# Kernel optimization log

Hardware: AMD Instinct MI355X
Metric: run time of the kernel (lower is better)

## Reference

```python
import jax, jax.numpy as jnp
import numpy as np

STRIDE = 2
PADDING = (1, 1)
OUT_PADDING = (0, 0)


def conv_transpose2d(x, weight, bias, stride, padding, out_padding):
    # weight: (Cin, Cout, kh, kw) -- torch ConvTranspose2d layout.
    # The original code does: stride-insert zeros, zero-pad by (k-1), append
    # out_padding rows/cols, valid-conv with the spatially-flipped kernel,
    # then crop `padding` from each side. That is exactly a dilated conv:
    kh, kw = weight.shape[2], weight.shape[3]
    w = jnp.flip(weight, (2, 3)).transpose(1, 0, 2, 3)  # (Cout, Cin, kh, kw)
    pad = ((kh - 1 - padding[0], kh - 1 - padding[0] + out_padding[0]),
           (kw - 1 - padding[1], kw - 1 - padding[1] + out_padding[1]))
    out = jax.lax.conv_general_dilated(
        x, w,
        window_strides=(1, 1),
        padding=pad,
        lhs_dilation=(stride, stride),
        dimension_numbers=('NCHW', 'OIHW', 'NCHW'))
    return out + bias[None, :, None, None]


def setup_inputs() -> dict:
    key = jax.random.key(0)
    k1, k2, k3 = jax.random.split(key, 3)
    Cin, Cout, kh, kw = 256, 128, 4, 4
    bnd = (1.0 / (Cin * kh * kw)) ** 0.5  # matches uniform_(-k**0.5, k**0.5)
    x = jax.random.normal(k1, (16, Cin, 64, 64), dtype=jnp.float32)
    weight = jax.random.uniform(k2, (Cin, Cout, kh, kw), jnp.float32, -bnd, bnd)
    bias = jax.random.uniform(k3, (Cout,), jnp.float32, -bnd, bnd)
    return {"x": x, "weight": weight, "bias": bias}


def reference(x, weight, bias):
    # Output: (16, 128, 128, 128) = (H-1)*2 - 2*1 + 4
    return conv_transpose2d(x, weight, bias, STRIDE, PADDING, OUT_PADDING)
```

## Files before the change

### kernel.cpp

```cpp
#include <hip/hip_runtime.h>
#include <stdint.h>

typedef unsigned short u16;
typedef __bf16 bf16x8 __attribute__((ext_vector_type(8)));
typedef float f32x4 __attribute__((ext_vector_type(4)));

static const size_t XT_BYTES = (size_t)16 * 66 * 66 * 256 * 2;
static const size_t WK_BYTES = (size_t)2 * 4 * 8 * 2 * 128 * 32 * 2;

__device__ __forceinline__ u16 f2bf(float f) {
  unsigned u = __float_as_uint(f);
  unsigned r = (u + 0x7fff + ((u >> 16) & 1)) >> 16;
  return (u16)r;
}

__device__ __forceinline__ void ld_g2l16(const u16* g, void* l) {
  __builtin_amdgcn_global_load_lds(
      (const __attribute__((address_space(1))) unsigned int*)(uintptr_t)g,
      (__attribute__((address_space(3))) unsigned int*)(unsigned int)(uintptr_t)l,
      16, 0, 0);
}

__device__ __forceinline__ int swz4(int row) { return (row ^ (row >> 2)) & 3; }

__global__ __launch_bounds__(256) void prep_x(const float* __restrict__ x,
                                              u16* __restrict__ xt) {
  __shared__ __align__(16) u16 sh[64 * 264];
  const int t = threadIdx.x;
  const int ihp = blockIdx.x;
  const int n = blockIdx.y;
  u16* xtn = xt + ((size_t)(n * 66 + ihp)) * 66 * 256;
  if (ihp == 0 || ihp == 65) {
    for (int j = 0; j < 9; ++j) {
      int idx = j * 256 + t;
      if (idx < 2112) ((uint4*)xtn)[idx] = make_uint4(0, 0, 0, 0);
    }
    return;
  }
  const int ih = ihp - 1;
  const int iw0 = (t & 15) * 4;
  const int cib = t >> 4;
  const float* xb = x + (size_t)n * 1048576 + (size_t)ih * 64;
#pragma unroll
  for (int it = 0; it < 16; ++it) {
    int ci = it * 16 + cib;
    const float4 v = *(const float4*)(xb + (size_t)ci * 4096 + iw0);
    sh[(iw0 + 0) * 264 + ci] = f2bf(v.x);
    sh[(iw0 + 1) * 264 + ci] = f2bf(v.y);
    sh[(iw0 + 2) * 264 + ci] = f2bf(v.z);
    sh[(iw0 + 3) * 264 + ci] = f2bf(v.w);
  }
  __syncthreads();
#pragma unroll
  for (int j = 0; j < 8; ++j) {
    int idx = j * 256 + t;
    int iw = idx >> 5;
    int chunk = idx & 31;
    uint4 v = *(const uint4*)&sh[iw * 264 + chunk * 8];
    *(uint4*)&xtn[(size_t)(iw + 1) * 256 + chunk * 8] = v;
  }
  if (t < 64) {
    int iwp = (t >> 5) * 65;
    int chunk = t & 31;
    *(uint4*)&xtn[(size_t)iwp * 256 + chunk * 8] = make_uint4(0, 0, 0, 0);
  }
}

__global__ __launch_bounds__(256) void prep_w(const float* __restrict__ w,
                                              u16* __restrict__ wk) {
  int id = blockIdx.x * 256 + threadIdx.x;
  int ci5 = id & 31;
  int co = (id >> 5) & 127;
  int q = (id >> 12) & 1;
  int kc = (id >> 13) & 7;
  int tap = (id >> 16) & 3;
  int p = id >> 18;
  int ci = kc * 32 + ci5;
  int dh = tap >> 1, dw = tap & 1;
  int kh = 2 * dh + 1 - p;
  int kw = 2 * dw + 1 - q;
  wk[id] = f2bf(w[((ci * 128 + co) * 4 + kh) * 4 + kw]);
}

__global__ __launch_bounds__(256, 2) void gemm_ct(const u16* __restrict__ xt,
                                                  const u16* __restrict__ wk,
                                                  const float* __restrict__ bias,
                                                  float* __restrict__ out) {
  __shared__ __align__(16) u16 As[2][8192];
  __shared__ __align__(16) u16 Bs[2][4224];
  const int t = threadIdx.x;
  const int lane = t & 63;
  const int wv = t >> 6;
  const int wm = wv >> 1, wn = wv & 1;
  const int quad = lane >> 4, l15 = lane & 15;

  const int id = blockIdx.x;
  const int sid = (id & 7) * 128 + (id >> 3);
  const int mt = sid & 31;
  const int n = (sid >> 5) & 15;
  const int p = sid >> 9;
  const int m0 = mt * 2;

  const u16* wkp = wk + (size_t)p * 262144;
  const u16* xtn = xt + (size_t)n * (66 * 66 * 256);

  int aoffs[4];
#pragma unroll
  for (int it = 0; it < 4; ++it) {
    int c = it * 256 + t;
    int co = (c >> 2) & 127;
    aoffs[it] = (c >> 2) * 32 + ((c & 3) ^ swz4(co)) * 8;
  }
  int bsrc[3];
#pragma unroll
  for (int it = 0; it < 3; ++it) {
    int c = it * 256 + t;
    int r = (c >= 264) ? 1 : 0;
    int rem = c - 264 * r;
    int iwp = rem >> 2;
    bsrc[it] = r * 16896 + iwp * 256 + ((rem & 3) ^ swz4(iwp)) * 8;
  }

  int aro[2][4];
#pragma unroll
  for (int q = 0; q < 2; ++q)
#pragma unroll
    for (int i = 0; i < 4; ++i) {
      int co = wm * 64 + i * 16 + l15;
      aro[q][i] = (q * 128 + co) * 32 + (quad ^ swz4(co)) * 8;
    }
  int bro0[4], bro1[4], bro2[4];
#pragma unroll
  for (int j = 0; j < 4; ++j) {
    int b0 = j * 16 + l15;
    bro0[j] = wn * 2112 + b0 * 32 + (quad ^ swz4(b0)) * 8;
    bro1[j] = wn * 2112 + (b0 + 1) * 32 + (quad ^ swz4(b0 + 1)) * 8;
    bro2[j] = wn * 2112 + (b0 + 2) * 32 + (quad ^ swz4(b0 + 2)) * 8;
  }

  f32x4 acc[2][4][4];
#pragma unroll
  for (int q = 0; q < 2; ++q)
#pragma unroll
    for (int i = 0; i < 4; ++i)
#pragma unroll
      for (int j = 0; j < 4; ++j) acc[q][i][j] = (f32x4){0.f, 0.f, 0.f, 0.f};

  const int mpp1 = m0 + p + 1;

  auto stage = [&](int buf, int s) {
    const u16* asrc = wkp + (size_t)s * 8192;
    u16* Ad = &As[buf][0];
    u16* Bd = &Bs[buf][0];
#pragma unroll
    for (int it = 0; it < 4; ++it)
      ld_g2l16(asrc + aoffs[it], Ad + (it * 256 + t) * 8);
    const int dh = s >> 4;
    const u16* bbase = xtn + (size_t)(mpp1 - dh) * 16896 + (s & 7) * 32;
    ld_g2l16(bbase + bsrc[0], Bd + t * 8);
    ld_g2l16(bbase + bsrc[1], Bd + (256 + t) * 8);
    if (t < 16) ld_g2l16(bbase + bsrc[2], Bd + (512 + t) * 8);
  };

  stage(0, 0);
  asm volatile("s_waitcnt vmcnt(0)" ::: "memory");
  __builtin_amdgcn_s_barrier();
  asm volatile("" ::: "memory");

  int cur = 0;
  for (int s = 0; s < 32; ++s) {
    if (s + 1 < 32) stage(cur ^ 1, s + 1);
    const int dw = (s >> 3) & 1;
    int brq0[4], brq1[4];
#pragma unroll
    for (int j = 0; j < 4; ++j) {
      brq0[j] = dw ? bro0[j] : bro1[j];
      brq1[j] = dw ? bro1[j] : bro2[j];
    }
    const u16* Ac = &As[cur][0];
    const u16* Bc = &Bs[cur][0];
    {
      bf16x8 af0[4], bf0[4];
#pragma unroll
      for (int i = 0; i < 4; ++i) af0[i] = *(const bf16x8*)(Ac + aro[0][i]);
#pragma unroll
      for (int j = 0; j < 4; ++j) bf0[j] = *(const bf16x8*)(Bc + brq0[j]);
      __builtin_amdgcn_s_setprio(1);
#pragma unroll
      for (int i = 0; i < 4; ++i)
#pragma unroll
        for (int j = 0; j < 4; ++j)
          acc[0][i][j] = __builtin_amdgcn_mfma_f32_16x16x32_bf16(
              af0[i], bf0[j], acc[0][i][j], 0, 0, 0);
      __builtin_amdgcn_s_setprio(0);
      bf16x8 af1[4], bf1[4];
#pragma unroll
      for (int i = 0; i < 4; ++i) af1[i] = *(const bf16x8*)(Ac + aro[1][i]);
#pragma unroll
      for (int j = 0; j < 4; ++j) bf1[j] = *(const bf16x8*)(Bc + brq1[j]);
      __builtin_amdgcn_s_setprio(1);
#pragma unroll
      for (int i = 0; i < 4; ++i)
#pragma unroll
        for (int j = 0; j < 4; ++j)
          acc[1][i][j] = __builtin_amdgcn_mfma_f32_16x16x32_bf16(
              af1[i], bf1[j], acc[1][i][j], 0, 0, 0);
      __builtin_amdgcn_s_setprio(0);
    }
    asm volatile("s_waitcnt lgkmcnt(0) vmcnt(0)" ::: "memory");
    __builtin_amdgcn_s_barrier();
    asm volatile("" ::: "memory");
    cur ^= 1;
  }

  const int oh = 2 * (m0 + wn) + p;
  float bv[4][4];
#pragma unroll
  for (int i = 0; i < 4; ++i)
#pragma unroll
    for (int r = 0; r < 4; ++r) bv[i][r] = bias[wm * 64 + i * 16 + quad * 4 + r];
#pragma unroll
  for (int i = 0; i < 4; ++i)
#pragma unroll
    for (int j = 0; j < 4; ++j) {
      int l = j * 16 + l15;
#pragma unroll
      for (int r = 0; r < 4; ++r) {
        int co = wm * 64 + i * 16 + quad * 4 + r;
        float2 v;
        v.x = acc[0][i][j][r] + bv[i][r];
        v.y = acc[1][i][j][r] + bv[i][r];
        *(float2*)&out[(((size_t)n * 128 + co) * 128 + oh) * 128 + 2 * l] = v;
      }
    }
}

__global__ __launch_bounds__(256) void ct_fallback(const float* __restrict__ x,
                                                   const float* __restrict__ w,
                                                   const float* __restrict__ bias,
                                                   float* __restrict__ out) {
  size_t id = (size_t)blockIdx.x * 256 + threadIdx.x;
  if (id >= (size_t)16 * 128 * 128 * 128) return;
  int ow = (int)(id & 127), oh = (int)(id >> 7) & 127;
  int co = (int)(id >> 14) & 127, n = (int)(id >> 21);
  int pp = oh & 1, m = oh >> 1, qq = ow & 1, l = ow >> 1;
  float s = bias[co];
  for (int ci = 0; ci < 256; ++ci) {
    for (int dh = 0; dh < 2; ++dh) {
      int ih = m + pp - dh;
      if (ih < 0 || ih > 63) continue;
      int kh = 2 * dh + 1 - pp;
      for (int dw = 0; dw < 2; ++dw) {
        int iw = l + qq - dw;
        if (iw < 0 || iw > 63) continue;
        int kw = 2 * dw + 1 - qq;
        s += x[(((size_t)n * 256 + ci) * 64 + ih) * 64 + iw] *
             w[((ci * 128 + co) * 4 + kh) * 4 + kw];
      }
    }
  }
  out[id] = s;
}

extern "C" void kernel_launch(void* const* d_in, const int* in_sizes, int n_in,
                              void* d_out, int out_size, void* d_ws, size_t ws_size,
                              hipStream_t stream) {
  const float* x = (const float*)d_in[0];
  const float* w = (const float*)d_in[1];
  const float* bias = (const float*)d_in[2];
  float* out = (float*)d_out;
  if (ws_size >= XT_BYTES + WK_BYTES) {
    u16* xt = (u16*)d_ws;
    u16* wkb = (u16*)((char*)d_ws + XT_BYTES);
    hipLaunchKernelGGL(prep_x, dim3(66, 16), dim3(256), 0, stream, x, xt);
    hipLaunchKernelGGL(prep_w, dim3(2048), dim3(256), 0, stream, w, wkb);
    hipLaunchKernelGGL(gemm_ct, dim3(1024), dim3(256), 0, stream, xt, wkb, bias, out);
  } else {
    hipLaunchKernelGGL(ct_fallback, dim3(131072), dim3(256), 0, stream, x, w, bias, out);
  }
}
```

Baseline: 260.5 us.

## Reorder weight taps to reuse B fragments across dw pairs and vectorize prep

Weights are re-laid out so the two dw taps for a given (dh, kc) sit next to each other. The main loop now processes pairs of stages that share one B tile, which halves B global loads and lets the middle B fragment stay in registers across both halves. A and B staging are decoupled with split vmcnt waits, and there are now two barriers per pair. The prep_x transpose writes ushort4 into an XOR-swizzled LDS layout to cut bank conflicts and scalar stores. The epilogue uses nontemporal output stores.

```diff
diff --git a/kernel.cpp b/kernel.cpp
--- a/kernel.cpp
+++ b/kernel.cpp
@@ -4,9 +4,10 @@
 typedef unsigned short u16;
 typedef __bf16 bf16x8 __attribute__((ext_vector_type(8)));
 typedef float f32x4 __attribute__((ext_vector_type(4)));
+typedef float f32x2 __attribute__((ext_vector_type(2)));
 
 static const size_t XT_BYTES = (size_t)16 * 66 * 66 * 256 * 2;
-static const size_t WK_BYTES = (size_t)2 * 4 * 8 * 2 * 128 * 32 * 2;
+static const size_t WK_BYTES = (size_t)2 * 2 * 8 * 2 * 2 * 128 * 32 * 2;
 
 __device__ __forceinline__ u16 f2bf(float f) {
   unsigned u = __float_as_uint(f);
@@ -39,16 +40,26 @@
   }
   const int ih = ihp - 1;
   const int iw0 = (t & 15) * 4;
-  const int cib = t >> 4;
-  const float* xb = x + (size_t)n * 1048576 + (size_t)ih * 64;
-#pragma unroll
-  for (int it = 0; it < 16; ++it) {
-    int ci = it * 16 + cib;
-    const float4 v = *(const float4*)(xb + (size_t)ci * 4096 + iw0);
-    sh[(iw0 + 0) * 264 + ci] = f2bf(v.x);
-    sh[(iw0 + 1) * 264 + ci] = f2bf(v.y);
-    sh[(iw0 + 2) * 264 + ci] = f2bf(v.z);
-    sh[(iw0 + 3) * 264 + ci] = f2bf(v.w);
+  const int cb = (t >> 4) * 4;
+  const int swz = (t & 3) << 3;
+  const float* xb = x + (size_t)n * 1048576 + (size_t)ih * 64 + iw0;
+#pragma unroll
+  for (int it = 0; it < 4; ++it) {
+    int ci0 = it * 64 + cb;
+    float4 v0 = *(const float4*)(xb + (size_t)(ci0 + 0) * 4096);
+    float4 v1 = *(const float4*)(xb + (size_t)(ci0 + 1) * 4096);
+    float4 v2 = *(const float4*)(xb + (size_t)(ci0 + 2) * 4096);
+    float4 v3 = *(const float4*)(xb + (size_t)(ci0 + 3) * 4096);
+    int col = ci0 ^ swz;
+    ushort4 u;
+    u.x = f2bf(v0.x); u.y = f2bf(v1.x); u.z = f2bf(v2.x); u.w = f2bf(v3.x);
+    *(ushort4*)&sh[(iw0 + 0) * 264 + col] = u;
+    u.x = f2bf(v0.y); u.y = f2bf(v1.y); u.z = f2bf(v2.y); u.w = f2bf(v3.y);
+    *(ushort4*)&sh[(iw0 + 1) * 264 + col] = u;
+    u.x = f2bf(v0.z); u.y = f2bf(v1.z); u.z = f2bf(v2.z); u.w = f2bf(v3.z);
+    *(ushort4*)&sh[(iw0 + 2) * 264 + col] = u;
+    u.x = f2bf(v0.w); u.y = f2bf(v1.w); u.z = f2bf(v2.w); u.w = f2bf(v3.w);
+    *(ushort4*)&sh[(iw0 + 3) * 264 + col] = u;
   }
   __syncthreads();
 #pragma unroll
@@ -56,7 +67,7 @@
     int idx = j * 256 + t;
     int iw = idx >> 5;
     int chunk = idx & 31;
-    uint4 v = *(const uint4*)&sh[iw * 264 + chunk * 8];
+    uint4 v = *(const uint4*)&sh[iw * 264 + ((chunk ^ ((iw >> 2) & 3)) << 3)];
     *(uint4*)&xtn[(size_t)(iw + 1) * 256 + chunk * 8] = v;
   }
   if (t < 64) {
@@ -72,11 +83,11 @@
   int ci5 = id & 31;
   int co = (id >> 5) & 127;
   int q = (id >> 12) & 1;
-  int kc = (id >> 13) & 7;
-  int tap = (id >> 16) & 3;
+  int dw = (id >> 13) & 1;
+  int kc = (id >> 14) & 7;
+  int dh = (id >> 17) & 1;
   int p = id >> 18;
   int ci = kc * 32 + ci5;
-  int dh = tap >> 1, dw = tap & 1;
   int kh = 2 * dh + 1 - p;
   int kw = 2 * dw + 1 - q;
   wk[id] = f2bf(w[((ci * 128 + co) * 4 + kh) * 4 + kw]);
@@ -129,14 +140,14 @@
       int co = wm * 64 + i * 16 + l15;
       aro[q][i] = (q * 128 + co) * 32 + (quad ^ swz4(co)) * 8;
     }
-  int bro0[4], bro1[4], bro2[4];
-#pragma unroll
-  for (int j = 0; j < 4; ++j) {
-    int b0 = j * 16 + l15;
-    bro0[j] = wn * 2112 + b0 * 32 + (quad ^ swz4(b0)) * 8;
-    bro1[j] = wn * 2112 + (b0 + 1) * 32 + (quad ^ swz4(b0 + 1)) * 8;
-    bro2[j] = wn * 2112 + (b0 + 2) * 32 + (quad ^ swz4(b0 + 2)) * 8;
-  }
+  int bro[3][4];
+#pragma unroll
+  for (int k = 0; k < 3; ++k)
+#pragma unroll
+    for (int j = 0; j < 4; ++j) {
+      int b0 = j * 16 + l15 + k;
+      bro[k][j] = wn * 2112 + b0 * 32 + (quad ^ swz4(b0)) * 8;
+    }
 
   f32x4 acc[2][4][4];
 #pragma unroll
@@ -148,91 +159,127 @@
 
   const int mpp1 = m0 + p + 1;
 
-  auto stage = [&](int buf, int s) {
+  auto stageA = [&](int buf, int s) {
     const u16* asrc = wkp + (size_t)s * 8192;
     u16* Ad = &As[buf][0];
-    u16* Bd = &Bs[buf][0];
 #pragma unroll
     for (int it = 0; it < 4; ++it)
       ld_g2l16(asrc + aoffs[it], Ad + (it * 256 + t) * 8);
-    const int dh = s >> 4;
-    const u16* bbase = xtn + (size_t)(mpp1 - dh) * 16896 + (s & 7) * 32;
+  };
+  auto stageB = [&](int buf, int pr) {
+    const int kc = pr & 7, dh = pr >> 3;
+    const u16* bbase = xtn + (size_t)(mpp1 - dh) * 16896 + kc * 32;
+    u16* Bd = &Bs[buf][0];
     ld_g2l16(bbase + bsrc[0], Bd + t * 8);
     ld_g2l16(bbase + bsrc[1], Bd + (256 + t) * 8);
     if (t < 16) ld_g2l16(bbase + bsrc[2], Bd + (512 + t) * 8);
   };
 
-  stage(0, 0);
+  stageA(0, 0);
+  stageB(0, 0);
   asm volatile("s_waitcnt vmcnt(0)" ::: "memory");
   __builtin_amdgcn_s_barrier();
   asm volatile("" ::: "memory");
 
-  int cur = 0;
-  for (int s = 0; s < 32; ++s) {
-    if (s + 1 < 32) stage(cur ^ 1, s + 1);
-    const int dw = (s >> 3) & 1;
-    int brq0[4], brq1[4];
-#pragma unroll
-    for (int j = 0; j < 4; ++j) {
-      brq0[j] = dw ? bro0[j] : bro1[j];
-      brq1[j] = dw ? bro1[j] : bro2[j];
-    }
-    const u16* Ac = &As[cur][0];
-    const u16* Bc = &Bs[cur][0];
+  bf16x8 keep[4];
+#pragma unroll 1
+  for (int pr = 0; pr < 16; ++pr) {
+    const u16* Bc = &Bs[pr & 1][0];
     {
-      bf16x8 af0[4], bf0[4];
-#pragma unroll
-      for (int i = 0; i < 4; ++i) af0[i] = *(const bf16x8*)(Ac + aro[0][i]);
-#pragma unroll
-      for (int j = 0; j < 4; ++j) bf0[j] = *(const bf16x8*)(Bc + brq0[j]);
+      stageA(1, 2 * pr + 1);
+      __builtin_amdgcn_sched_barrier(0);
+      if (pr < 15) stageB((pr + 1) & 1, pr + 1);
+      __builtin_amdgcn_sched_barrier(0);
+      const u16* Ac = &As[0][0];
+      bf16x8 a0[4];
+#pragma unroll
+      for (int i = 0; i < 4; ++i) a0[i] = *(const bf16x8*)(Ac + aro[0][i]);
+#pragma unroll
+      for (int j = 0; j < 4; ++j) keep[j] = *(const bf16x8*)(Bc + bro[1][j]);
       __builtin_amdgcn_s_setprio(1);
 #pragma unroll
       for (int i = 0; i < 4; ++i)
 #pragma unroll
         for (int j = 0; j < 4; ++j)
           acc[0][i][j] = __builtin_amdgcn_mfma_f32_16x16x32_bf16(
-              af0[i], bf0[j], acc[0][i][j], 0, 0, 0);
+              a0[i], keep[j], acc[0][i][j], 0, 0, 0);
       __builtin_amdgcn_s_setprio(0);
-      bf16x8 af1[4], bf1[4];
-#pragma unroll
-      for (int i = 0; i < 4; ++i) af1[i] = *(const bf16x8*)(Ac + aro[1][i]);
-#pragma unroll
-      for (int j = 0; j < 4; ++j) bf1[j] = *(const bf16x8*)(Bc + brq1[j]);
+      bf16x8 a1[4], b2[4];
+#pragma unroll
+      for (int i = 0; i < 4; ++i) a1[i] = *(const bf16x8*)(Ac + aro[1][i]);
+#pragma unroll
+      for (int j = 0; j < 4; ++j) b2[j] = *(const bf16x8*)(Bc + bro[2][j]);
       __builtin_amdgcn_s_setprio(1);
 #pragma unroll
       for (int i = 0; i < 4; ++i)
 #pragma unroll
         for (int j = 0; j < 4; ++j)
           acc[1][i][j] = __builtin_amdgcn_mfma_f32_16x16x32_bf16(
-              af1[i], bf1[j], acc[1][i][j], 0, 0, 0);
+              a1[i], b2[j], acc[1][i][j], 0, 0, 0);
       __builtin_amdgcn_s_setprio(0);
-    }
-    asm volatile("s_waitcnt lgkmcnt(0) vmcnt(0)" ::: "memory");
-    __builtin_amdgcn_s_barrier();
-    asm volatile("" ::: "memory");
-    cur ^= 1;
+      if (pr < 15) {
+        if (wv == 0)
+          asm volatile("s_waitcnt lgkmcnt(0) vmcnt(3)" ::: "memory");
+        else
+          asm volatile("s_waitcnt lgkmcnt(0) vmcnt(2)" ::: "memory");
+      } else {
+        asm volatile("s_waitcnt lgkmcnt(0) vmcnt(0)" ::: "memory");
+      }
+      __builtin_amdgcn_s_barrier();
+      asm volatile("" ::: "memory");
+    }
+    {
+      if (pr < 15) stageA(0, 2 * pr + 2);
+      __builtin_amdgcn_sched_barrier(0);
+      const u16* Ac = &As[1][0];
+      bf16x8 a0[4], b0[4];
+#pragma unroll
+      for (int i = 0; i < 4; ++i) a0[i] = *(const bf16x8*)(Ac + aro[0][i]);
+#pragma unroll
+      for (int j = 0; j < 4; ++j) b0[j] = *(const bf16x8*)(Bc + bro[0][j]);
+      __builtin_amdgcn_s_setprio(1);
+#pragma unroll
+      for (int i = 0; i < 4; ++i)
+#pragma unroll
+        for (int j = 0; j < 4; ++j)
+          acc[0][i][j] = __builtin_amdgcn_mfma_f32_16x16x32_bf16(
+              a0[i], b0[j], acc[0][i][j], 0, 0, 0);
+      __builtin_amdgcn_s_setprio(0);
+      bf16x8 a1[4];
+#pragma unroll
+      for (int i = 0; i < 4; ++i) a1[i] = *(const bf16x8*)(Ac + aro[1][i]);
+      __builtin_amdgcn_s_setprio(1);
+#pragma unroll
+      for (int i = 0; i < 4; ++i)
+#pragma unroll
+        for (int j = 0; j < 4; ++j)
+          acc[1][i][j] = __builtin_amdgcn_mfma_f32_16x16x32_bf16(
+              a1[i], keep[j], acc[1][i][j], 0, 0, 0);
+      __builtin_amdgcn_s_setprio(0);
+      asm volatile("s_waitcnt lgkmcnt(0) vmcnt(0)" ::: "memory");
+      __builtin_amdgcn_s_barrier();
+      asm volatile("" ::: "memory");
+    }
   }
 
   const int oh = 2 * (m0 + wn) + p;
-  float bv[4][4];
-#pragma unroll
-  for (int i = 0; i < 4; ++i)
-#pragma unroll
-    for (int r = 0; r < 4; ++r) bv[i][r] = bias[wm * 64 + i * 16 + quad * 4 + r];
-#pragma unroll
-  for (int i = 0; i < 4; ++i)
+#pragma unroll
+  for (int i = 0; i < 4; ++i) {
 #pragma unroll
     for (int j = 0; j < 4; ++j) {
       int l = j * 16 + l15;
 #pragma unroll
       for (int r = 0; r < 4; ++r) {
         int co = wm * 64 + i * 16 + quad * 4 + r;
-        float2 v;
-        v.x = acc[0][i][j][r] + bv[i][r];
-        v.y = acc[1][i][j][r] + bv[i][r];
-        *(float2*)&out[(((size_t)n * 128 + co) * 128 + oh) * 128 + 2 * l] = v;
+        float bv = bias[co];
+        f32x2 v;
+        v.x = acc[0][i][j][r] + bv;
+        v.y = acc[1][i][j][r] + bv;
+        __builtin_nontemporal_store(
+            v, (f32x2*)&out[(((size_t)n * 128 + co) * 128 + oh) * 128 + 2 * l]);
       }
     }
+  }
 }
 
 __global__ __launch_bounds__(256) void ct_fallback(const float* __restrict__ x,
```

Measured after the change: 246.3 us. 1.06x faster.
